# Performance work log

Measured on AMD Instinct MI355X. Metric: run time of the kernel, lower is better.

Reference implementation:

```python
import jax, jax.numpy as jnp
import numpy as np

E = 1_000_000
C_IN = 11
H = 64
N_LAYERS = 4
LN_EPS = 1e-5


def setup_inputs() -> dict:
    key = jax.random.key(0)
    ks = jax.random.split(key, 12)
    x = jax.random.normal(ks[0], (E, C_IN), dtype=jnp.float32)
    neighbors = jax.random.randint(ks[1], (E, 4), 0, E)
    s0 = 1.0 / np.sqrt(5 * C_IN)
    s1 = 1.0 / np.sqrt(5 * H)
    w0 = jax.random.uniform(ks[2], (5 * C_IN, H), jnp.float32, -s0, s0)
    b0 = jax.random.uniform(ks[3], (H,), jnp.float32, -s0, s0)
    w_rest = jax.random.uniform(ks[4], (N_LAYERS - 1, 5 * H, H), jnp.float32, -s1, s1)
    b_rest = jax.random.uniform(ks[5], (N_LAYERS - 1, H), jnp.float32, -s1, s1)
    ln_g = jnp.ones((N_LAYERS, H), jnp.float32)
    ln_b = jnp.zeros((N_LAYERS, H), jnp.float32)
    sc1 = 1.0 / np.sqrt(H)
    sc2 = 1.0 / np.sqrt(H // 2)
    cw1 = jax.random.uniform(ks[6], (H, H // 2), jnp.float32, -sc1, sc1)
    cb1 = jax.random.uniform(ks[7], (H // 2,), jnp.float32, -sc1, sc1)
    cw2 = jax.random.uniform(ks[8], (H // 2, 1), jnp.float32, -sc2, sc2)
    cb2 = jax.random.uniform(ks[9], (1,), jnp.float32, -sc2, sc2)
    return {"x": x, "neighbors": neighbors, "w0": w0, "b0": b0,
            "w_rest": w_rest, "b_rest": b_rest, "ln_g": ln_g, "ln_b": ln_b,
            "cw1": cw1, "cb1": cb1, "cw2": cw2, "cb2": cb2}


def _mesh_conv(x, neighbors, W, b):
    # Gather 4-ring neighbor features: [E,4,C]
    n = x[neighbors]
    a, bb, c, d = n[:, 0], n[:, 1], n[:, 2], n[:, 3]
    # Symmetric MeshCNN features -> 5*C, then linear projection.
    feats = jnp.concatenate([x, jnp.abs(a - c), a + c, jnp.abs(bb - d), bb + d], axis=-1)
    return feats @ W + b


def _layernorm(h, g, b):
    mu = jnp.mean(h, axis=-1, keepdims=True)
    var = jnp.var(h, axis=-1, keepdims=True)
    return (h - mu) * jax.lax.rsqrt(var + LN_EPS) * g + b


def reference(x, neighbors, w0, b0, w_rest, b_rest, ln_g, ln_b, cw1, cb1, cw2, cb2):
    # Layer 0 (no residual; dropout is identity in eval mode)
    h = jax.nn.relu(_layernorm(_mesh_conv(x, neighbors, w0, b0), ln_g[0], ln_b[0]))
    x = h
    for i in range(1, N_LAYERS):
        h = _mesh_conv(x, neighbors, w_rest[i - 1], b_rest[i - 1])
        h = jax.nn.relu(_layernorm(h, ln_g[i], ln_b[i]))
        x = h + x  # residual from layer 2 onward (shapes match)
    z = jax.nn.relu(x @ cw1 + cb1)
    logits = (z @ cw2 + cb2).squeeze(-1)
    return logits
```

## Files before the change

### kernel.cpp

```cpp
#include <hip/hip_runtime.h>
#include <hip/hip_bf16.h>
#include <math.h>

#define E_EDGES 1000000
#define LN_EPS  1e-5f

typedef unsigned short u16;
typedef __bf16 bf16x8 __attribute__((ext_vector_type(8)));
typedef float  f32x16 __attribute__((ext_vector_type(16)));

__device__ __forceinline__ float lo2f(unsigned d) {
    union { unsigned u; float f; } v; v.u = d << 16; return v.f;
}
__device__ __forceinline__ float hi2f(unsigned d) {
    union { unsigned u; float f; } v; v.u = d & 0xffff0000u; return v.f;
}
__device__ __forceinline__ float bf2f(u16 u) {
    union { unsigned u; float f; } v; v.u = ((unsigned)u) << 16; return v.f;
}
__device__ __forceinline__ unsigned pk2(float lo, float hi) {
    __hip_bfloat162 h = __float22bfloat162_rn(make_float2(lo, hi));
    unsigned r; __builtin_memcpy(&r, &h, 4); return r;
}

__global__ __launch_bounds__(256) void wconv_kernel(
    const float* __restrict__ wr, const float* __restrict__ w0,
    const float* __restrict__ cw1, u16* __restrict__ wf)
{
    const int s = blockIdx.x * 256 + threadIdx.x;
    if (s >= 8448) return;
    const int l    = s & 63;
    const int half = l >> 5;
    uint4 pk;
    if (s < 3 * 2560) {
        const int col = ((s >> 6) & 1) * 32 + (l & 31);
        const int L  = s / 2560;
        const int sl = s % 2560;
        const int kb = (sl >> 7) * 16 + half * 8;
        const float* W = wr + L * 320 * 64;
        pk.x = pk2(W[(kb+0)*64+col], W[(kb+1)*64+col]);
        pk.y = pk2(W[(kb+2)*64+col], W[(kb+3)*64+col]);
        pk.z = pk2(W[(kb+4)*64+col], W[(kb+5)*64+col]);
        pk.w = pk2(W[(kb+6)*64+col], W[(kb+7)*64+col]);
    } else if (s < 8192) {
        const int col = ((s >> 6) & 1) * 32 + (l & 31);
        const int sl = s - 3 * 2560;
        const int kb = (sl >> 7) * 16 + half * 8;
        float v[8];
        #pragma unroll
        for (int p = 0; p < 8; ++p) v[p] = (kb + p < 55) ? w0[(kb+p)*64 + col] : 0.f;
        pk.x = pk2(v[0],v[1]); pk.y = pk2(v[2],v[3]);
        pk.z = pk2(v[4],v[5]); pk.w = pk2(v[6],v[7]);
    } else {
        const int sl = s - 8192;
        const int ks = sl >> 6;
        const int col = l & 31;
        const int kb = ks * 16 + half * 8;
        pk.x = pk2(cw1[(kb+0)*32+col], cw1[(kb+1)*32+col]);
        pk.y = pk2(cw1[(kb+2)*32+col], cw1[(kb+3)*32+col]);
        pk.z = pk2(cw1[(kb+4)*32+col], cw1[(kb+5)*32+col]);
        pk.w = pk2(cw1[(kb+6)*32+col], cw1[(kb+7)*32+col]);
    }
    *(uint4*)&wf[(size_t)s * 8] = pk;
}

__global__ __launch_bounds__(256) void xprep_kernel(
    const float* __restrict__ x, u16* __restrict__ xc)
{
    __shared__ float xs[2816];
    const int t = threadIdx.x;
    const long long i0 = (long long)blockIdx.x * 704;
    #pragma unroll
    for (int k = 0; k < 3; ++k) {
        const int idx = t + k * 256;
        if (idx < 704 && i0 + idx < 2750000)
            *(float4*)&xs[idx * 4] = ((const float4*)x)[i0 + idx];
    }
    __syncthreads();
    const size_t e = (size_t)blockIdx.x * 256 + t;
    if (e < E_EDGES) {
        const float* r = &xs[t * 11];
        uint4 o0, o1;
        o0.x = pk2(r[0], r[1]);  o0.y = pk2(r[2], r[3]);
        o0.z = pk2(r[4], r[5]);  o0.w = pk2(r[6], r[7]);
        o1.x = pk2(r[8], r[9]);  o1.y = pk2(r[10], 0.f);
        o1.z = 0u;               o1.w = 0u;
        *(uint4*)&xc[e * 16]     = o0;
        *(uint4*)&xc[e * 16 + 8] = o1;
    }
}

__global__ __launch_bounds__(256, 4) void layer0_mfma(
    const u16* __restrict__ xc, const int* __restrict__ nbr,
    const u16* __restrict__ wf0, const float* __restrict__ bias,
    const float* __restrict__ lng, const float* __restrict__ lnb,
    u16* __restrict__ xout)
{
    __shared__ float smem[64 * 68];
    __shared__ u16  raw[64 * 5 * 16];
    u16* afrag = (u16*)smem;
    const int t  = threadIdx.x;
    const int l  = t & 63;
    const int wv = t >> 6;
    const int e0 = blockIdx.x * 64;
    const int el = t >> 2, cq = t & 3;

    {
        const size_t e = (size_t)(e0 + el);
        const int4 n = *(const int4*)(nbr + 4 * e);
        const int nj = (cq == 0) ? n.x : (cq == 1) ? n.y : (cq == 2) ? n.z : n.w;
        const u16* nr = xc + (size_t)nj * 16;
        u16* dst = raw + (el * 5 + 1 + cq) * 16;
        *(uint4*)dst       = *(const uint4*)nr;
        *(uint4*)(dst + 8) = *(const uint4*)(nr + 8);
        if (cq == 0) {
            const u16* xr = xc + e * 16;
            u16* od = raw + (el * 5) * 16;
            *(uint4*)od       = *(const uint4*)xr;
            *(uint4*)(od + 8) = *(const uint4*)(xr + 8);
        }
    }
    __syncthreads();

    {
        const u16* R = raw + el * 5 * 16;
        float f[16];
        if (cq == 0) {
            #pragma unroll
            for (int i = 0; i < 11; ++i) f[i] = bf2f(R[i]);
            #pragma unroll
            for (int i = 0; i < 5; ++i) f[11+i] = fabsf(bf2f(R[16+i]) - bf2f(R[48+i]));
        } else if (cq == 1) {
            #pragma unroll
            for (int i = 0; i < 6; ++i) f[i] = fabsf(bf2f(R[16+5+i]) - bf2f(R[48+5+i]));
            #pragma unroll
            for (int i = 0; i < 10; ++i) f[6+i] = bf2f(R[16+i]) + bf2f(R[48+i]);
        } else if (cq == 2) {
            f[0] = bf2f(R[16+10]) + bf2f(R[48+10]);
            #pragma unroll
            for (int i = 0; i < 11; ++i) f[1+i] = fabsf(bf2f(R[32+i]) - bf2f(R[64+i]));
            #pragma unroll
            for (int i = 0; i < 4; ++i) f[12+i] = bf2f(R[32+i]) + bf2f(R[64+i]);
        } else {
            #pragma unroll
            for (int i = 0; i < 7; ++i) f[i] = bf2f(R[32+4+i]) + bf2f(R[64+4+i]);
            #pragma unroll
            for (int i = 7; i < 16; ++i) f[i] = 0.f;
        }
        const int mt_g  = el >> 5;
        const int lane0 = el & 31;
        u16* abase = afrag + (size_t)mt_g * (4 * 64 * 8);
        #pragma unroll
        for (int hh = 0; hh < 2; ++hh) {
            uint4 pk;
            pk.x = pk2(f[hh*8+0], f[hh*8+1]);
            pk.y = pk2(f[hh*8+2], f[hh*8+3]);
            pk.z = pk2(f[hh*8+4], f[hh*8+5]);
            pk.w = pk2(f[hh*8+6], f[hh*8+7]);
            const int gsw = (lane0 + 32 * hh) ^ cq;
            *(uint4*)(abase + (size_t)(cq * 64 + gsw) * 8) = pk;
        }
    }
    __syncthreads();

    const int mt = wv >> 1, nt = wv & 1;
    f32x16 acc = {};
    const u16* ab = afrag + (size_t)mt * (4 * 512);
    const u16* bb = wf0 + (size_t)(nt * 64 + l) * 8;
    #pragma unroll
    for (int ks = 0; ks < 4; ++ks) {
        const bf16x8 a8 = *(const bf16x8*)(ab + (size_t)(ks * 64 + (l ^ ks)) * 8);
        const bf16x8 b8 = *(const bf16x8*)(bb + ks * 1024);
        acc = __builtin_amdgcn_mfma_f32_32x32x16_bf16(a8, b8, acc, 0, 0, 0);
    }
    __syncthreads();

    float* ebuf = smem;
    {
        const int col  = nt * 32 + (l & 31);
        const int quad = l >> 5;
        const float bc = bias[col];
        #pragma unroll
        for (int r = 0; r < 16; ++r) {
            const int row = mt * 32 + (r & 3) + 8 * (r >> 2) + 4 * quad;
            ebuf[row * 68 + col] = acc[r] + bc;
        }
    }
    __syncthreads();

    {
        const float* rp = ebuf + el * 68 + cq * 16;
        float v[16];
        float s = 0.f, qs = 0.f;
        #pragma unroll
        for (int i = 0; i < 16; ++i) { v[i] = rp[i]; s += v[i]; qs += v[i] * v[i]; }
        s  += __shfl_xor(s, 1);  s  += __shfl_xor(s, 2);
        qs += __shfl_xor(qs, 1); qs += __shfl_xor(qs, 2);
        const float mu   = s * (1.f / 64.f);
        const float var  = qs * (1.f / 64.f) - mu * mu;
        const float rinv = rsqrtf(var + LN_EPS);
        const size_t e   = (size_t)(e0 + el);
        u16* outp        = xout + e * 64 + cq * 16;
        #pragma unroll
        for (int h = 0; h < 2; ++h) {
            uint4 o; unsigned* op = (unsigned*)&o;
            #pragma unroll
            for (int i = 0; i < 4; ++i) {
                const int ci = cq * 16 + h * 8 + i * 2;
                const float y0 = fmaxf(fmaf((v[h*8+i*2]   - mu) * rinv, lng[ci],   lnb[ci]),   0.f);
                const float y1 = fmaxf(fmaf((v[h*8+i*2+1] - mu) * rinv, lng[ci+1], lnb[ci+1]), 0.f);
                op[i] = pk2(y0, y1);
            }
            *(uint4*)(outp + h * 8) = o;
        }
    }
}

__device__ __forceinline__ void layer_gather_pack(
    const u16* __restrict__ xin, const int* __restrict__ nbr,
    u16* __restrict__ afrag, int e0, int el, int cq, uint4& xv0, uint4& xv1)
{
    const size_t e = (size_t)(e0 + el);
    const int4 n = *(const int4*)(nbr + 4 * e);
    const u16* xr = xin + e * 64           + cq * 16;
    const u16* ar = xin + (size_t)n.x * 64 + cq * 16;
    const u16* br = xin + (size_t)n.y * 64 + cq * 16;
    const u16* cr = xin + (size_t)n.z * 64 + cq * 16;
    const u16* dr = xin + (size_t)n.w * 64 + cq * 16;
    xv0 = *(const uint4*)(xr);                 xv1 = *(const uint4*)(xr + 8);
    const uint4 av0 = *(const uint4*)(ar);     const uint4 av1 = *(const uint4*)(ar + 8);
    const uint4 bv0 = *(const uint4*)(br);     const uint4 bv1 = *(const uint4*)(br + 8);
    const uint4 cv0 = *(const uint4*)(cr);     const uint4 cv1 = *(const uint4*)(cr + 8);
    const uint4 dv0 = *(const uint4*)(dr);     const uint4 dv1 = *(const uint4*)(dr + 8);
    const int mt_g  = el >> 5;
    const int lane0 = el & 31;
    u16* abase = afrag + (size_t)mt_g * (20 * 64 * 8);
    #pragma unroll
    for (int w8 = 0; w8 < 2; ++w8) {
        const uint4 xv = w8 ? xv1 : xv0;
        const uint4 av = w8 ? av1 : av0;
        const uint4 bv = w8 ? bv1 : bv0;
        const uint4 cv = w8 ? cv1 : cv0;
        const uint4 dv = w8 ? dv1 : dv0;
        const int gsw = (lane0 + 32 * w8) ^ cq;
        uint4 g1, g2, g3, g4;
        const unsigned* ap = (const unsigned*)&av;
        const unsigned* bp = (const unsigned*)&bv;
        const unsigned* cp = (const unsigned*)&cv;
        const unsigned* dp = (const unsigned*)&dv;
        unsigned* g1p = (unsigned*)&g1; unsigned* g2p = (unsigned*)&g2;
        unsigned* g3p = (unsigned*)&g3; unsigned* g4p = (unsigned*)&g4;
        #pragma unroll
        for (int i = 0; i < 4; ++i) {
            const float a0 = lo2f(ap[i]), a1 = hi2f(ap[i]);
            const float c0 = lo2f(cp[i]), c1 = hi2f(cp[i]);
            g1p[i] = pk2(a0 - c0, a1 - c1) & 0x7FFF7FFFu;
            g2p[i] = pk2(a0 + c0, a1 + c1);
            const float b0 = lo2f(bp[i]), b1 = hi2f(bp[i]);
            const float d0 = lo2f(dp[i]), d1 = hi2f(dp[i]);
            g3p[i] = pk2(b0 - d0, b1 - d1) & 0x7FFF7FFFu;
            g4p[i] = pk2(b0 + d0, b1 + d1);
        }
        *(uint4*)(abase + (size_t)(((0*4 + cq) * 64) + gsw) * 8) = xv;
        *(uint4*)(abase + (size_t)(((1*4 + cq) * 64) + gsw) * 8) = g1;
        *(uint4*)(abase + (size_t)(((2*4 + cq) * 64) + gsw) * 8) = g2;
        *(uint4*)(abase + (size_t)(((3*4 + cq) * 64) + gsw) * 8) = g3;
        *(uint4*)(abase + (size_t)(((4*4 + cq) * 64) + gsw) * 8) = g4;
    }
}

__global__ __launch_bounds__(256, 4) void layer_mfma(
    const u16* __restrict__ xin, const int* __restrict__ nbr,
    const u16* __restrict__ wf, const float* __restrict__ bias,
    const float* __restrict__ lng, const float* __restrict__ lnb,
    u16* __restrict__ xout)
{
    __shared__ u16 afrag[2 * 20 * 64 * 8];
    const int t  = threadIdx.x;
    const int l  = t & 63;
    const int wv = t >> 6;
    const int e0 = blockIdx.x * 64;
    const int el = t >> 2;
    const int cq = t & 3;

    float lgv[16], lbv[16];
    #pragma unroll
    for (int j = 0; j < 4; ++j) {
        *(float4*)&lgv[j * 4] = *(const float4*)(lng + cq * 16 + j * 4);
        *(float4*)&lbv[j * 4] = *(const float4*)(lnb + cq * 16 + j * 4);
    }

    uint4 xv0, xv1;
    layer_gather_pack(xin, nbr, afrag, e0, el, cq, xv0, xv1);
    __syncthreads();

    const int mt = wv >> 1, nt = wv & 1;
    f32x16 acc = {};
    const u16* ab = afrag + (size_t)mt * (20 * 512);
    const u16* bb = wf + (size_t)(nt * 64 + l) * 8;
    #pragma unroll
    for (int ks = 0; ks < 20; ++ks) {
        const bf16x8 a8 = *(const bf16x8*)(ab + (size_t)(ks * 64 + (l ^ (ks & 3))) * 8);
        const bf16x8 b8 = *(const bf16x8*)(bb + ks * 1024);
        acc = __builtin_amdgcn_mfma_f32_32x32x16_bf16(a8, b8, acc, 0, 0, 0);
    }
    __syncthreads();

    float* ebuf = (float*)afrag;
    {
        const int col  = nt * 32 + (l & 31);
        const int quad = l >> 5;
        const float bc = bias[col];
        #pragma unroll
        for (int r = 0; r < 16; ++r) {
            const int row = mt * 32 + (r & 3) + 8 * (r >> 2) + 4 * quad;
            ebuf[row * 68 + col] = acc[r] + bc;
        }
    }
    __syncthreads();

    {
        const float* rp = ebuf + el * 68 + cq * 16;
        float v[16];
        float s = 0.f, qs = 0.f;
        #pragma unroll
        for (int i = 0; i < 16; ++i) { v[i] = rp[i]; s += v[i]; qs += v[i] * v[i]; }
        s  += __shfl_xor(s, 1);  s  += __shfl_xor(s, 2);
        qs += __shfl_xor(qs, 1); qs += __shfl_xor(qs, 2);
        const float mu   = s * (1.f / 64.f);
        const float var  = qs * (1.f / 64.f) - mu * mu;
        const float rinv = rsqrtf(var + LN_EPS);
        const size_t e   = (size_t)(e0 + el);
        u16* outp        = xout + e * 64 + cq * 16;
        #pragma unroll
        for (int h = 0; h < 2; ++h) {
            const uint4 res = h ? xv1 : xv0;
            const unsigned* rr = (const unsigned*)&res;
            uint4 o; unsigned* op = (unsigned*)&o;
            #pragma unroll
            for (int i = 0; i < 4; ++i) {
                const int k = h * 8 + i * 2;
                const float y0 = fmaxf(fmaf((v[k]   - mu) * rinv, lgv[k],   lbv[k]),   0.f) + lo2f(rr[i]);
                const float y1 = fmaxf(fmaf((v[k+1] - mu) * rinv, lgv[k+1], lbv[k+1]), 0.f) + hi2f(rr[i]);
                op[i] = pk2(y0, y1);
            }
            *(uint4*)(outp + h * 8) = o;
        }
    }
}

__global__ __launch_bounds__(256, 4) void layer_head_mfma(
    const u16* __restrict__ xin, const int* __restrict__ nbr,
    const u16* __restrict__ wf, const float* __restrict__ bias,
    const float* __restrict__ lng, const float* __restrict__ lnb,
    const u16* __restrict__ wfh, const float* __restrict__ cb1,
    const float* __restrict__ cw2, const float* __restrict__ cb2,
    float* __restrict__ out)
{
    __shared__ u16 afrag[2 * 20 * 64 * 8];
    u16*   ybuf  = afrag + 9216;
    float* hbuf2 = (float*)(afrag + 14336);
    const int t  = threadIdx.x;
    const int l  = t & 63;
    const int wv = t >> 6;
    const int e0 = blockIdx.x * 64;
    const int el = t >> 2;
    const int cq = t & 3;

    float lgv[16], lbv[16];
    #pragma unroll
    for (int j = 0; j < 4; ++j) {
        *(float4*)&lgv[j * 4] = *(const float4*)(lng + cq * 16 + j * 4);
        *(float4*)&lbv[j * 4] = *(const float4*)(lnb + cq * 16 + j * 4);
    }

    uint4 xv0, xv1;
    layer_gather_pack(xin, nbr, afrag, e0, el, cq, xv0, xv1);
    __syncthreads();

    const int mt = wv >> 1, nt = wv & 1;
    f32x16 acc = {};
    {
        const u16* ab = afrag + (size_t)mt * (20 * 512);
        const u16* bb = wf + (size_t)(nt * 64 + l) * 8;
        #pragma unroll
        for (int ks = 0; ks < 20; ++ks) {
            const bf16x8 a8 = *(const bf16x8*)(ab + (size_t)(ks * 64 + (l ^ (ks & 3))) * 8);
            const bf16x8 b8 = *(const bf16x8*)(bb + ks * 1024);
            acc = __builtin_amdgcn_mfma_f32_32x32x16_bf16(a8, b8, acc, 0, 0, 0);
        }
    }
    __syncthreads();

    float* ebuf = (float*)afrag;
    {
        const int col  = nt * 32 + (l & 31);
        const int quad = l >> 5;
        const float bc = bias[col];
        #pragma unroll
        for (int r = 0; r < 16; ++r) {
            const int row = mt * 32 + (r & 3) + 8 * (r >> 2) + 4 * quad;
            ebuf[row * 68 + col] = acc[r] + bc;
        }
    }
    __syncthreads();

    {
        const float* rp = ebuf + el * 68 + cq * 16;
        float v[16];
        float s = 0.f, qs = 0.f;
        #pragma unroll
        for (int i = 0; i < 16; ++i) { v[i] = rp[i]; s += v[i]; qs += v[i] * v[i]; }
        s  += __shfl_xor(s, 1);  s  += __shfl_xor(s, 2);
        qs += __shfl_xor(qs, 1); qs += __shfl_xor(qs, 2);
        const float mu   = s * (1.f / 64.f);
        const float var  = qs * (1.f / 64.f) - mu * mu;
        const float rinv = rsqrtf(var + LN_EPS);
        const int mt_g  = el >> 5;
        const int lane0 = el & 31;
        #pragma unroll
        for (int h = 0; h < 2; ++h) {
            const uint4 res = h ? xv1 : xv0;
            const unsigned* rr = (const unsigned*)&res;
            uint4 o; unsigned* op = (unsigned*)&o;
            #pragma unroll
            for (int i = 0; i < 4; ++i) {
                const int k = h * 8 + i * 2;
                const float y0 = fmaxf(fmaf((v[k]   - mu) * rinv, lgv[k],   lbv[k]),   0.f) + lo2f(rr[i]);
                const float y1 = fmaxf(fmaf((v[k+1] - mu) * rinv, lgv[k+1], lbv[k+1]), 0.f) + hi2f(rr[i]);
                op[i] = pk2(y0, y1);
            }
            const int gsw = (lane0 + 32 * h) ^ cq;
            *(uint4*)(ybuf + (size_t)(((mt_g * 4 + cq) * 64) + gsw) * 8) = o;
        }
    }
    __syncthreads();

    if (wv < 2) {
        const int mt2 = wv;
        f32x16 a2 = {};
        #pragma unroll
        for (int ks = 0; ks < 4; ++ks) {
            const bf16x8 a8 = *(const bf16x8*)(ybuf + (size_t)(((mt2 * 4 + ks) * 64) + (l ^ ks)) * 8);
            const bf16x8 b8 = *(const bf16x8*)(wfh + (size_t)(ks * 64 + l) * 8);
            a2 = __builtin_amdgcn_mfma_f32_32x32x16_bf16(a8, b8, a2, 0, 0, 0);
        }
        const int col = l & 31;
        const float bc1 = cb1[col];
        const float w2v = cw2[col];
        float* hb = hbuf2 + mt2 * (32 * 33);
        #pragma unroll
        for (int r = 0; r < 16; ++r) {
            const int row = (r & 3) + 8 * (r >> 2) + 4 * (l >> 5);
            hb[row * 33 + col] = fmaxf(a2[r] + bc1, 0.f) * w2v;
        }
    }
    __syncthreads();

    if (t < 128) {
        const int edge = t >> 1, part = t & 1;
        const float* rp = hbuf2 + (edge >> 5) * (32 * 33) + (edge & 31) * 33 + part * 16;
        float s = 0.f;
        #pragma unroll
        for (int i = 0; i < 16; ++i) s += rp[i];
        s += __shfl_xor(s, 1);
        if (part == 0) out[e0 + edge] = s + cb2[0];
    }
}

__global__ __launch_bounds__(256) void head_mfma(
    const u16* __restrict__ xin,
    const float* __restrict__ cw1, const float* __restrict__ cb1,
    const float* __restrict__ cw2, const float* __restrict__ cb2,
    float* __restrict__ out)
{
    __shared__ float hbuf[4][32 * 33];
    const int t    = threadIdx.x;
    const int l    = t & 63;
    const int wv   = t >> 6;
    const int col  = l & 31;
    const int half = l >> 5;

    bf16x8 bf[4];
    #pragma unroll
    for (int ks = 0; ks < 4; ++ks) {
        const int kb = ks * 16 + half * 8;
        uint4 pk;
        pk.x = pk2(cw1[(kb+0)*32 + col], cw1[(kb+1)*32 + col]);
        pk.y = pk2(cw1[(kb+2)*32 + col], cw1[(kb+3)*32 + col]);
        pk.z = pk2(cw1[(kb+4)*32 + col], cw1[(kb+5)*32 + col]);
        pk.w = pk2(cw1[(kb+6)*32 + col], cw1[(kb+7)*32 + col]);
        __builtin_memcpy(&bf[ks], &pk, 16);
    }
    const float bc = cb1[col];
    const float w2 = cw2[col];
    const float b2 = cb2[0];

    int tile = blockIdx.x * 4 + wv;
    const int valid = tile < (E_EDGES / 32);
    if (!valid) tile = E_EDGES / 32 - 1;
    const size_t e0 = (size_t)tile * 32;
    const u16* xb = xin + (e0 + col) * 64 + half * 8;
    f32x16 acc = {};
    #pragma unroll
    for (int ks = 0; ks < 4; ++ks) {
        const bf16x8 a8 = *(const bf16x8*)(xb + ks * 16);
        acc = __builtin_amdgcn_mfma_f32_32x32x16_bf16(a8, bf[ks], acc, 0, 0, 0);
    }
    float* hb = hbuf[wv];
    #pragma unroll
    for (int r = 0; r < 16; ++r) {
        const int row = (r & 3) + 8 * (r >> 2) + 4 * half;
        hb[row * 33 + col] = fmaxf(acc[r] + bc, 0.f) * w2;
    }
    __syncthreads();
    const int row2 = l >> 1, part = l & 1;
    const float* rp = hb + row2 * 33 + part * 16;
    float s = 0.f;
    #pragma unroll
    for (int i = 0; i < 16; ++i) s += rp[i];
    s += __shfl_xor(s, 1);
    if (valid && part == 0) out[e0 + row2] = s + b2;
}

extern "C" void kernel_launch(void* const* d_in, const int* in_sizes, int n_in,
                              void* d_out, int out_size, void* d_ws, size_t ws_size,
                              hipStream_t stream)
{
// ... 41 lines not shown
```

Measured before the change: 645.1 us.

## Make each wave own 16 edges with 16x16x32 MFMA and wave-local sync

Restructures the mesh-conv layer kernels so that each wavefront processes its own 16 edges end to end. Each wave keeps a private LDS slice and computes all 64 output columns with 16x16x32 bf16 MFMAs instead of four waves sharing 32x32 tiles. Block-wide __syncthreads are replaced by wave-local lgkmcnt waits, and the weight prepacking is reordered to the new fragment layout. The head reduction now uses cross-lane shuffles instead of an LDS pass. This removes inter-wave barrier stalls. In exchange, every wave reloads the full weight fragments from global memory and the XOR LDS swizzle is dropped, so bank conflicts may appear.

```diff
diff --git a/kernel.cpp b/kernel.cpp
--- a/kernel.cpp
+++ b/kernel.cpp
@@ -7,7 +7,13 @@
 
 typedef unsigned short u16;
 typedef __bf16 bf16x8 __attribute__((ext_vector_type(8)));
-typedef float  f32x16 __attribute__((ext_vector_type(16)));
+typedef float  f32x4  __attribute__((ext_vector_type(4)));
+
+#define WAVE_SYNC() do {                                      \
+    __builtin_amdgcn_sched_barrier(0);                        \
+    asm volatile("s_waitcnt lgkmcnt(0)" ::: "memory");        \
+    __builtin_amdgcn_sched_barrier(0);                        \
+} while (0)
 
 __device__ __forceinline__ float lo2f(unsigned d) {
     union { unsigned u; float f; } v; v.u = d << 16; return v.f;
@@ -30,36 +36,42 @@
     const int s = blockIdx.x * 256 + threadIdx.x;
     if (s >= 8448) return;
     const int l    = s & 63;
-    const int half = l >> 5;
+    const int colb = l & 15;
+    const int k0   = (l >> 4) * 8;
     uint4 pk;
     if (s < 3 * 2560) {
-        const int col = ((s >> 6) & 1) * 32 + (l & 31);
         const int L  = s / 2560;
         const int sl = s % 2560;
-        const int kb = (sl >> 7) * 16 + half * 8;
+        const int ks = sl >> 8;
+        const int nt = (sl >> 6) & 3;
+        const int k  = 32 * ks + k0;
+        const int col = nt * 16 + colb;
         const float* W = wr + L * 320 * 64;
-        pk.x = pk2(W[(kb+0)*64+col], W[(kb+1)*64+col]);
-        pk.y = pk2(W[(kb+2)*64+col], W[(kb+3)*64+col]);
-        pk.z = pk2(W[(kb+4)*64+col], W[(kb+5)*64+col]);
-        pk.w = pk2(W[(kb+6)*64+col], W[(kb+7)*64+col]);
+        pk.x = pk2(W[(k+0)*64+col], W[(k+1)*64+col]);
+        pk.y = pk2(W[(k+2)*64+col], W[(k+3)*64+col]);
+        pk.z = pk2(W[(k+4)*64+col], W[(k+5)*64+col]);
+        pk.w = pk2(W[(k+6)*64+col], W[(k+7)*64+col]);
     } else if (s < 8192) {
-        const int col = ((s >> 6) & 1) * 32 + (l & 31);
         const int sl = s - 3 * 2560;
-        const int kb = (sl >> 7) * 16 + half * 8;
+        const int ks = sl >> 8;
+        const int nt = (sl >> 6) & 3;
+        const int k  = 32 * ks + k0;
+        const int col = nt * 16 + colb;
         float v[8];
         #pragma unroll
-        for (int p = 0; p < 8; ++p) v[p] = (kb + p < 55) ? w0[(kb+p)*64 + col] : 0.f;
+        for (int p = 0; p < 8; ++p) v[p] = (k + p < 55) ? w0[(k+p)*64 + col] : 0.f;
         pk.x = pk2(v[0],v[1]); pk.y = pk2(v[2],v[3]);
         pk.z = pk2(v[4],v[5]); pk.w = pk2(v[6],v[7]);
     } else {
         const int sl = s - 8192;
-        const int ks = sl >> 6;
-        const int col = l & 31;
-        const int kb = ks * 16 + half * 8;
-        pk.x = pk2(cw1[(kb+0)*32+col], cw1[(kb+1)*32+col]);
-        pk.y = pk2(cw1[(kb+2)*32+col], cw1[(kb+3)*32+col]);
-        pk.z = pk2(cw1[(kb+4)*32+col], cw1[(kb+5)*32+col]);
-        pk.w = pk2(cw1[(kb+6)*32+col], cw1[(kb+7)*32+col]);
+        const int ks = sl >> 7;
+        const int nt = (sl >> 6) & 1;
+        const int k  = 32 * ks + k0;
+        const int col = nt * 16 + colb;
+        pk.x = pk2(cw1[(k+0)*32+col], cw1[(k+1)*32+col]);
+        pk.y = pk2(cw1[(k+2)*32+col], cw1[(k+3)*32+col]);
+        pk.z = pk2(cw1[(k+4)*32+col], cw1[(k+5)*32+col]);
+        pk.w = pk2(cw1[(k+6)*32+col], cw1[(k+7)*32+col]);
     }
     *(uint4*)&wf[(size_t)s * 8] = pk;
 }
@@ -96,17 +108,17 @@
     const float* __restrict__ lng, const float* __restrict__ lnb,
     u16* __restrict__ xout)
 {
-    __shared__ float smem[64 * 68];
-    __shared__ u16  raw[64 * 5 * 16];
-    u16* afrag = (u16*)smem;
+    __shared__ u16 lds[4 * 2304];
     const int t  = threadIdx.x;
     const int l  = t & 63;
     const int wv = t >> 6;
-    const int e0 = blockIdx.x * 64;
-    const int el = t >> 2, cq = t & 3;
-
-    {
-        const size_t e = (size_t)(e0 + el);
+    u16* raw = lds + wv * 2304;
+    u16* aw  = raw + 1280;
+    const int el = l >> 2, cq = l & 3;
+    const int e0w = blockIdx.x * 64 + wv * 16;
+
+    {
+        const size_t e = (size_t)e0w + el;
         const int4 n = *(const int4*)(nbr + 4 * e);
         const int nj = (cq == 0) ? n.x : (cq == 1) ? n.y : (cq == 2) ? n.z : n.w;
         const u16* nr = xc + (size_t)nj * 16;
@@ -115,15 +127,15 @@
         *(uint4*)(dst + 8) = *(const uint4*)(nr + 8);
         if (cq == 0) {
             const u16* xr = xc + e * 16;
-            u16* od = raw + (el * 5) * 16;
+            u16* od = raw + el * 5 * 16;
             *(uint4*)od       = *(const uint4*)xr;
-            *(uint4*)(od + 8) = *(const uint4*)(xr + 8);
-        }
-    }
-    __syncthreads();
-
-    {
-        const u16* R = raw + el * 5 * 16;
+            *(uint4*)(od + 8) = *(const uint4*)(nr - nr + xr + 8);
+        }
+    }
+    WAVE_SYNC();
+
+    {
+        const u16* R = raw + el * 80;
         float f[16];
         if (cq == 0) {
             #pragma unroll
@@ -147,49 +159,47 @@
             #pragma unroll
             for (int i = 7; i < 16; ++i) f[i] = 0.f;
         }
-        const int mt_g  = el >> 5;
-        const int lane0 = el & 31;
-        u16* abase = afrag + (size_t)mt_g * (4 * 64 * 8);
-        #pragma unroll
-        for (int hh = 0; hh < 2; ++hh) {
+        const int base = (cq >> 1) * 64 + (cq & 1) * 32 + el;
+        #pragma unroll
+        for (int h = 0; h < 2; ++h) {
             uint4 pk;
-            pk.x = pk2(f[hh*8+0], f[hh*8+1]);
-            pk.y = pk2(f[hh*8+2], f[hh*8+3]);
-            pk.z = pk2(f[hh*8+4], f[hh*8+5]);
-            pk.w = pk2(f[hh*8+6], f[hh*8+7]);
-            const int gsw = (lane0 + 32 * hh) ^ cq;
-            *(uint4*)(abase + (size_t)(cq * 64 + gsw) * 8) = pk;
-        }
-    }
-    __syncthreads();
-
-    const int mt = wv >> 1, nt = wv & 1;
-    f32x16 acc = {};
-    const u16* ab = afrag + (size_t)mt * (4 * 512);
-    const u16* bb = wf0 + (size_t)(nt * 64 + l) * 8;
-    #pragma unroll
-    for (int ks = 0; ks < 4; ++ks) {
-        const bf16x8 a8 = *(const bf16x8*)(ab + (size_t)(ks * 64 + (l ^ ks)) * 8);
-        const bf16x8 b8 = *(const bf16x8*)(bb + ks * 1024);
-        acc = __builtin_amdgcn_mfma_f32_32x32x16_bf16(a8, b8, acc, 0, 0, 0);
-    }
-    __syncthreads();
-
-    float* ebuf = smem;
-    {
-        const int col  = nt * 32 + (l & 31);
-        const int quad = l >> 5;
-        const float bc = bias[col];
-        #pragma unroll
-        for (int r = 0; r < 16; ++r) {
-            const int row = mt * 32 + (r & 3) + 8 * (r >> 2) + 4 * quad;
-            ebuf[row * 68 + col] = acc[r] + bc;
-        }
-    }
-    __syncthreads();
-
-    {
-        const float* rp = ebuf + el * 68 + cq * 16;
+            pk.x = pk2(f[h*8+0], f[h*8+1]);
+            pk.y = pk2(f[h*8+2], f[h*8+3]);
+            pk.z = pk2(f[h*8+4], f[h*8+5]);
+            pk.w = pk2(f[h*8+6], f[h*8+7]);
+            *(uint4*)(aw + (size_t)(base + h * 16) * 8) = pk;
+        }
+    }
+    WAVE_SYNC();
+
+    f32x4 ac0 = {}, ac1 = {}, ac2 = {}, ac3 = {};
+    #pragma unroll
+    for (int ks = 0; ks < 2; ++ks) {
+        const bf16x8 a8 = *(const bf16x8*)(aw + (size_t)(ks * 64 + l) * 8);
+        const u16* bk = wf0 + (size_t)(ks * 256 + l) * 8;
+        ac0 = __builtin_amdgcn_mfma_f32_16x16x32_bf16(a8, *(const bf16x8*)(bk       ), ac0, 0, 0, 0);
+        ac1 = __builtin_amdgcn_mfma_f32_16x16x32_bf16(a8, *(const bf16x8*)(bk +  512), ac1, 0, 0, 0);
+        ac2 = __builtin_amdgcn_mfma_f32_16x16x32_bf16(a8, *(const bf16x8*)(bk + 1024), ac2, 0, 0, 0);
+        ac3 = __builtin_amdgcn_mfma_f32_16x16x32_bf16(a8, *(const bf16x8*)(bk + 1536), ac3, 0, 0, 0);
+    }
+    WAVE_SYNC();
+
+    float* ew = (float*)raw;
+    const int colb = l & 15, rb = (l >> 4) * 4;
+    {
+        const float b0 = bias[colb],      b1 = bias[16 + colb];
+        const float b2 = bias[32 + colb], b3 = bias[48 + colb];
+        #pragma unroll
+        for (int r = 0; r < 4; ++r) {
+            float* er = ew + (rb + r) * 67;
+            er[colb]      = ac0[r] + b0;  er[16 + colb] = ac1[r] + b1;
+            er[32 + colb] = ac2[r] + b2;  er[48 + colb] = ac3[r] + b3;
+        }
+    }
+    WAVE_SYNC();
+
+    {
+        const float* rp = ew + el * 67 + cq * 16;
         float v[16];
         float s = 0.f, qs = 0.f;
         #pragma unroll
@@ -199,7 +209,7 @@
         const float mu   = s * (1.f / 64.f);
         const float var  = qs * (1.f / 64.f) - mu * mu;
         const float rinv = rsqrtf(var + LN_EPS);
-        const size_t e   = (size_t)(e0 + el);
+        const size_t e   = (size_t)e0w + el;
         u16* outp        = xout + e * 64 + cq * 16;
         #pragma unroll
         for (int h = 0; h < 2; ++h) {
@@ -216,11 +226,11 @@
     }
 }
 
-__device__ __forceinline__ void layer_gather_pack(
+__device__ __forceinline__ void gather_pack16(
     const u16* __restrict__ xin, const int* __restrict__ nbr,
-    u16* __restrict__ afrag, int e0, int el, int cq, uint4& xv0, uint4& xv1)
-{
-    const size_t e = (size_t)(e0 + el);
+    u16* __restrict__ aw, int e0w, int el, int cq, uint4& xv0, uint4& xv1)
+{
+    const size_t e = (size_t)e0w + el;
     const int4 n = *(const int4*)(nbr + 4 * e);
     const u16* xr = xin + e * 64           + cq * 16;
     const u16* ar = xin + (size_t)n.x * 64 + cq * 16;
@@ -232,17 +242,14 @@
     const uint4 bv0 = *(const uint4*)(br);     const uint4 bv1 = *(const uint4*)(br + 8);
     const uint4 cv0 = *(const uint4*)(cr);     const uint4 cv1 = *(const uint4*)(cr + 8);
     const uint4 dv0 = *(const uint4*)(dr);     const uint4 dv1 = *(const uint4*)(dr + 8);
-    const int mt_g  = el >> 5;
-    const int lane0 = el & 31;
-    u16* abase = afrag + (size_t)mt_g * (20 * 64 * 8);
-    #pragma unroll
-    for (int w8 = 0; w8 < 2; ++w8) {
-        const uint4 xv = w8 ? xv1 : xv0;
-        const uint4 av = w8 ? av1 : av0;
-        const uint4 bv = w8 ? bv1 : bv0;
-        const uint4 cv = w8 ? cv1 : cv0;
-        const uint4 dv = w8 ? dv1 : dv0;
-        const int gsw = (lane0 + 32 * w8) ^ cq;
+    const int base = (cq >> 1) * 64 + (cq & 1) * 32 + el;
+    #pragma unroll
+    for (int h = 0; h < 2; ++h) {
+        const uint4 xv = h ? xv1 : xv0;
+        const uint4 av = h ? av1 : av0;
+        const uint4 bv = h ? bv1 : bv0;
+        const uint4 cv = h ? cv1 : cv0;
+        const uint4 dv = h ? dv1 : dv0;
         uint4 g1, g2, g3, g4;
         const unsigned* ap = (const unsigned*)&av;
         const unsigned* bp = (const unsigned*)&bv;
@@ -261,11 +268,12 @@
             g3p[i] = pk2(b0 - d0, b1 - d1) & 0x7FFF7FFFu;
             g4p[i] = pk2(b0 + d0, b1 + d1);
         }
-        *(uint4*)(abase + (size_t)(((0*4 + cq) * 64) + gsw) * 8) = xv;
-        *(uint4*)(abase + (size_t)(((1*4 + cq) * 64) + gsw) * 8) = g1;
-        *(uint4*)(abase + (size_t)(((2*4 + cq) * 64) + gsw) * 8) = g2;
-        *(uint4*)(abase + (size_t)(((3*4 + cq) * 64) + gsw) * 8) = g3;
-        *(uint4*)(abase + (size_t)(((4*4 + cq) * 64) + gsw) * 8) = g4;
+        u16* w = aw + (size_t)(base + h * 16) * 8;
+        *(uint4*)(w)           = xv;
+        *(uint4*)(w + 128 * 8) = g1;
+        *(uint4*)(w + 256 * 8) = g2;
+        *(uint4*)(w + 384 * 8) = g3;
+        *(uint4*)(w + 512 * 8) = g4;
     }
 }
 
@@ -275,52 +283,52 @@
     const float* __restrict__ lng, const float* __restrict__ lnb,
     u16* __restrict__ xout)
 {
-    __shared__ u16 afrag[2 * 20 * 64 * 8];
+    __shared__ u16 lds[4 * 5120];
     const int t  = threadIdx.x;
     const int l  = t & 63;
     const int wv = t >> 6;
-    const int e0 = blockIdx.x * 64;
-    const int el = t >> 2;
-    const int cq = t & 3;
-
-    float lgv[16], lbv[16];
-    #pragma unroll
-    for (int j = 0; j < 4; ++j) {
-        *(float4*)&lgv[j * 4] = *(const float4*)(lng + cq * 16 + j * 4);
-        *(float4*)&lbv[j * 4] = *(const float4*)(lnb + cq * 16 + j * 4);
-    }
+    u16* aw = lds + wv * 5120;
+    const int el = l >> 2, cq = l & 3;
+    const int e0w = blockIdx.x * 64 + wv * 16;
 
     uint4 xv0, xv1;
-    layer_gather_pack(xin, nbr, afrag, e0, el, cq, xv0, xv1);
-    __syncthreads();
-
-    const int mt = wv >> 1, nt = wv & 1;
-    f32x16 acc = {};
-    const u16* ab = afrag + (size_t)mt * (20 * 512);
-    const u16* bb = wf + (size_t)(nt * 64 + l) * 8;
-    #pragma unroll
-    for (int ks = 0; ks < 20; ++ks) {
-        const bf16x8 a8 = *(const bf16x8*)(ab + (size_t)(ks * 64 + (l ^ (ks & 3))) * 8);
-        const bf16x8 b8 = *(const bf16x8*)(bb + ks * 1024);
-        acc = __builtin_amdgcn_mfma_f32_32x32x16_bf16(a8, b8, acc, 0, 0, 0);
-    }
-    __syncthreads();
-
-    float* ebuf = (float*)afrag;
-    {
-        const int col  = nt * 32 + (l & 31);
-        const int quad = l >> 5;
-        const float bc = bias[col];
-        #pragma unroll
-        for (int r = 0; r < 16; ++r) {
-            const int row = mt * 32 + (r & 3) + 8 * (r >> 2) + 4 * quad;
-            ebuf[row * 68 + col] = acc[r] + bc;
-        }
-    }
-    __syncthreads();
-
-    {
-        const float* rp = ebuf + el * 68 + cq * 16;
+    gather_pack16(xin, nbr, aw, e0w, el, cq, xv0, xv1);
+    WAVE_SYNC();
+
+    f32x4 ac0 = {}, ac1 = {}, ac2 = {}, ac3 = {};
+    #pragma unroll
+    for (int ks = 0; ks < 10; ++ks) {
+        const bf16x8 a8 = *(const bf16x8*)(aw + (size_t)(ks * 64 + l) * 8);
+        const u16* bk = wf + (size_t)(ks * 256 + l) * 8;
+        ac0 = __builtin_amdgcn_mfma_f32_16x16x32_bf16(a8, *(const bf16x8*)(bk       ), ac0, 0, 0, 0);
+        ac1 = __builtin_amdgcn_mfma_f32_16x16x32_bf16(a8, *(const bf16x8*)(bk +  512), ac1, 0, 0, 0);
+        ac2 = __builtin_amdgcn_mfma_f32_16x16x32_bf16(a8, *(const bf16x8*)(bk + 1024), ac2, 0, 0, 0);
+        ac3 = __builtin_amdgcn_mfma_f32_16x16x32_bf16(a8, *(const bf16x8*)(bk + 1536), ac3, 0, 0, 0);
+    }
+    WAVE_SYNC();
+
+    float* ew = (float*)aw;
+    const int colb = l & 15, rb = (l >> 4) * 4;
+    {
+        const float b0 = bias[colb],      b1 = bias[16 + colb];
+        const float b2 = bias[32 + colb], b3 = bias[48 + colb];
+        #pragma unroll
+        for (int r = 0; r < 4; ++r) {
+            float* er = ew + (rb + r) * 67;
+            er[colb]      = ac0[r] + b0;  er[16 + colb] = ac1[r] + b1;
+            er[32 + colb] = ac2[r] + b2;  er[48 + colb] = ac3[r] + b3;
+        }
+    }
+    WAVE_SYNC();
+
+    {
+        float lgv[16], lbv[16];
+        #pragma unroll
+        for (int j = 0; j < 4; ++j) {
+            *(float4*)&lgv[j * 4] = *(const float4*)(lng + cq * 16 + j * 4);
+            *(float4*)&lbv[j * 4] = *(const float4*)(lnb + cq * 16 + j * 4);
+        }
+        const float* rp = ew + el * 67 + cq * 16;
         float v[16];
         float s = 0.f, qs = 0.f;
         #pragma unroll
@@ -330,7 +338,7 @@
         const float mu   = s * (1.f / 64.f);
         const float var  = qs * (1.f / 64.f) - mu * mu;
         const float rinv = rsqrtf(var + LN_EPS);
-        const size_t e   = (size_t)(e0 + el);
+        const size_t e   = (size_t)e0w + el;
         u16* outp        = xout + e * 64 + cq * 16;
         #pragma unroll
         for (int h = 0; h < 2; ++h) {
@@ -357,56 +365,53 @@
     const float* __restrict__ cw2, const float* __restrict__ cb2,
     float* __restrict__ out)
 {
-    __shared__ u16 afrag[2 * 20 * 64 * 8];
-    u16*   ybuf  = afrag + 9216;
-    float* hbuf2 = (float*)(afrag + 14336);
+    __shared__ u16 lds[4 * 5120];
     const int t  = threadIdx.x;
     const int l  = t & 63;
     const int wv = t >> 6;
-    const int e0 = blockIdx.x * 64;
-    const int el = t >> 2;
-    const int cq = t & 3;
-
-    float lgv[16], lbv[16];
-    #pragma unroll
-    for (int j = 0; j < 4; ++j) {
-        *(float4*)&lgv[j * 4] = *(const float4*)(lng + cq * 16 + j * 4);
-        *(float4*)&lbv[j * 4] = *(const float4*)(lnb + cq * 16 + j * 4);
-    }
+    u16* aw = lds + wv * 5120;
+    u16* yb = aw + 2176;
+    const int el = l >> 2, cq = l & 3;
+    const int e0w = blockIdx.x * 64 + wv * 16;
 
     uint4 xv0, xv1;
-    layer_gather_pack(xin, nbr, afrag, e0, el, cq, xv0, xv1);
-    __syncthreads();
-
-    const int mt = wv >> 1, nt = wv & 1;
-    f32x16 acc = {};
-    {
-        const u16* ab = afrag + (size_t)mt * (20 * 512);
-        const u16* bb = wf + (size_t)(nt * 64 + l) * 8;
-        #pragma unroll
-        for (int ks = 0; ks < 20; ++ks) {
-            const bf16x8 a8 = *(const bf16x8*)(ab + (size_t)(ks * 64 + (l ^ (ks & 3))) * 8);
-            const bf16x8 b8 = *(const bf16x8*)(bb + ks * 1024);
-            acc = __builtin_amdgcn_mfma_f32_32x32x16_bf16(a8, b8, acc, 0, 0, 0);
-        }
-    }
-    __syncthreads();
-
-    float* ebuf = (float*)afrag;
-    {
-        const int col  = nt * 32 + (l & 31);
-        const int quad = l >> 5;
-        const float bc = bias[col];
-        #pragma unroll
-        for (int r = 0; r < 16; ++r) {
-            const int row = mt * 32 + (r & 3) + 8 * (r >> 2) + 4 * quad;
-            ebuf[row * 68 + col] = acc[r] + bc;
-        }
-    }
-    __syncthreads();
-
-    {
-        const float* rp = ebuf + el * 68 + cq * 16;
+    gather_pack16(xin, nbr, aw, e0w, el, cq, xv0, xv1);
+    WAVE_SYNC();
+
+    f32x4 ac0 = {}, ac1 = {}, ac2 = {}, ac3 = {};
+    #pragma unroll
+    for (int ks = 0; ks < 10; ++ks) {
+        const bf16x8 a8 = *(const bf16x8*)(aw + (size_t)(ks * 64 + l) * 8);
+        const u16* bk = wf + (size_t)(ks * 256 + l) * 8;
+        ac0 = __builtin_amdgcn_mfma_f32_16x16x32_bf16(a8, *(const bf16x8*)(bk       ), ac0, 0, 0, 0);
+        ac1 = __builtin_amdgcn_mfma_f32_16x16x32_bf16(a8, *(const bf16x8*)(bk +  512), ac1, 0, 0, 0);
+        ac2 = __builtin_amdgcn_mfma_f32_16x16x32_bf16(a8, *(const bf16x8*)(bk + 1024), ac2, 0, 0, 0);
+        ac3 = __builtin_amdgcn_mfma_f32_16x16x32_bf16(a8, *(const bf16x8*)(bk + 1536), ac3, 0, 0, 0);
+    }
+    WAVE_SYNC();
+
+    float* ew = (float*)aw;
+    const int colb = l & 15, rb = (l >> 4) * 4;
+    {
+        const float b0 = bias[colb],      b1 = bias[16 + colb];
+        const float b2 = bias[32 + colb], b3 = bias[48 + colb];
+        #pragma unroll
+        for (int r = 0; r < 4; ++r) {
+            float* er = ew + (rb + r) * 67;
+            er[colb]      = ac0[r] + b0;  er[16 + colb] = ac1[r] + b1;
+            er[32 + colb] = ac2[r] + b2;  er[48 + colb] = ac3[r] + b3;
+        }
+    }
+    WAVE_SYNC();
+
+    {
+        float lgv[16], lbv[16];
+        #pragma unroll
+        for (int j = 0; j < 4; ++j) {
+            *(float4*)&lgv[j * 4] = *(const float4*)(lng + cq * 16 + j * 4);
+            *(float4*)&lbv[j * 4] = *(const float4*)(lnb + cq * 16 + j * 4);
+        }
+        const float* rp = ew + el * 67 + cq * 16;
         float v[16];
         float s = 0.f, qs = 0.f;
         #pragma unroll
@@ -416,8 +421,7 @@
         const float mu   = s * (1.f / 64.f);
         const float var  = qs * (1.f / 64.f) - mu * mu;
         const float rinv = rsqrtf(var + LN_EPS);
-        const int mt_g  = el >> 5;
-        const int lane0 = el & 31;
+        const int ybase = (cq >> 1) * 64 + (cq & 1) * 32 + el;
         #pragma unroll
         for (int h = 0; h < 2; ++h) {
             const uint4 res = h ? xv1 : xv0;
@@ -430,41 +434,36 @@
                 const float y1 = fmaxf(fmaf((v[k+1] - mu) * rinv, lgv[k+1], lbv[k+1]), 0.f) + hi2f(rr[i]);
                 op[i] = pk2(y0, y1);
             }
-            const int gsw = (lane0 + 32 * h) ^ cq;
-            *(uint4*)(ybuf + (size_t)(((mt_g * 4 + cq) * 64) + gsw) * 8) = o;
-        }
-    }
-    __syncthreads();
-
-    if (wv < 2) {
-        const int mt2 = wv;
-        f32x16 a2 = {};
-        #pragma unroll
-        for (int ks = 0; ks < 4; ++ks) {
-            const bf16x8 a8 = *(const bf16x8*)(ybuf + (size_t)(((mt2 * 4 + ks) * 64) + (l ^ ks)) * 8);
-            const bf16x8 b8 = *(const bf16x8*)(wfh + (size_t)(ks * 64 + l) * 8);
-            a2 = __builtin_amdgcn_mfma_f32_32x32x16_bf16(a8, b8, a2, 0, 0, 0);
-        }
-        const int col = l & 31;
-        const float bc1 = cb1[col];
-        const float w2v = cw2[col];
-        float* hb = hbuf2 + mt2 * (32 * 33);
-        #pragma unroll
-        for (int r = 0; r < 16; ++r) {
-            const int row = (r & 3) + 8 * (r >> 2) + 4 * (l >> 5);
-            hb[row * 33 + col] = fmaxf(a2[r] + bc1, 0.f) * w2v;
-        }
-    }
-    __syncthreads();
-
-    if (t < 128) {
-        const int edge = t >> 1, part = t & 1;
-        const float* rp = hbuf2 + (edge >> 5) * (32 * 33) + (edge & 31) * 33 + part * 16;
-        float s = 0.f;
-        #pragma unroll
-        for (int i = 0; i < 16; ++i) s += rp[i];
-        s += __shfl_xor(s, 1);
-        if (part == 0) out[e0 + edge] = s + cb2[0];
+            *(uint4*)(yb + (size_t)(ybase + h * 16) * 8) = o;
+        }
+    }
+    WAVE_SYNC();
+
+    f32x4 h0 = {}, h1 = {};
+    #pragma unroll
+    for (int ks = 0; ks < 2; ++ks) {
+        const bf16x8 a8 = *(const bf16x8*)(yb + (size_t)(ks * 64 + l) * 8);
+        const u16* bk = wfh + (size_t)(ks * 128 + l) * 8;
+        h0 = __builtin_amdgcn_mfma_f32_16x16x32_bf16(a8, *(const bf16x8*)(bk      ), h0, 0, 0, 0);
+        h1 = __builtin_amdgcn_mfma_f32_16x16x32_bf16(a8, *(const bf16x8*)(bk + 512), h1, 0, 0, 0);
+    }
+    {
+        const float q1 = cb1[colb], q2 = cb1[16 + colb];
+        const float w1 = cw2[colb], w2 = cw2[16 + colb];
+        float sr[4];
+        #pragma unroll
+        for (int r = 0; r < 4; ++r)
+            sr[r] = fmaxf(h0[r] + q1, 0.f) * w1 + fmaxf(h1[r] + q2, 0.f) * w2;
+        #pragma unroll
+        for (int m = 1; m < 16; m <<= 1) {
+            #pragma unroll
+            for (int r = 0; r < 4; ++r) sr[r] += __shfl_xor(sr[r], m);
+        }
+        if (colb == 0) {
+            const float b2v = cb2[0];
+            #pragma unroll
+            for (int r = 0; r < 4; ++r) out[e0w + rb + r] = sr[r] + b2v;
+        }
     }
 }
 
@@ -474,6 +473,7 @@
     const float* __restrict__ cw2, const float* __restrict__ cb2,
     float* __restrict__ out)
 {
+    typedef float f32x16 __attribute__((ext_vector_type(16)));
     __shared__ float hbuf[4][32 * 33];
     const int t    = threadIdx.x;
     const int l    = t & 63;
```

Result: slower. 693.7 us (+7.5%).

## Split A-fragment staging into two K phases to shrink LDS footprint

Applied to the files above, without the earlier changes.

The layer kernels now stage the MFMA A operand in two phases: x plus the a/c features (12 k-steps) first, then the b/d features (8 k-steps) reuse the same shared buffer after a barrier. This cuts shared memory per block from 40 KB to about 24–25 KB, which may let more blocks reside per CU for this latency-bound gather workload. The LayerNorm gamma/beta loads are also moved to just before use to shorten register live ranges. In exchange there are two extra block barriers, and the b/d neighbor values stay live in registers across the first MFMA phase.

```diff
diff --git a/kernel.cpp b/kernel.cpp
--- a/kernel.cpp
+++ b/kernel.cpp
@@ -216,10 +216,37 @@
     }
 }
 
-__device__ __forceinline__ void layer_gather_pack(
+__device__ __forceinline__ void feat_pair(
+    const uint4 u, const uint4 w, uint4& gd, uint4& gs)
+{
+    const unsigned* up = (const unsigned*)&u;
+    const unsigned* wp = (const unsigned*)&w;
+    unsigned* dp = (unsigned*)&gd;
+    unsigned* sp = (unsigned*)&gs;
+    #pragma unroll
+    for (int i = 0; i < 4; ++i) {
+        const float u0 = lo2f(up[i]), u1 = hi2f(up[i]);
+        const float w0 = lo2f(wp[i]), w1 = hi2f(wp[i]);
+        dp[i] = pk2(u0 - w0, u1 - w1) & 0x7FFF7FFFu;
+        sp[i] = pk2(u0 + w0, u1 + w1);
+    }
+}
+
+__global__ __launch_bounds__(256, 4) void layer_mfma(
     const u16* __restrict__ xin, const int* __restrict__ nbr,
-    u16* __restrict__ afrag, int e0, int el, int cq, uint4& xv0, uint4& xv1)
-{
+    const u16* __restrict__ wf, const float* __restrict__ bias,
+    const float* __restrict__ lng, const float* __restrict__ lnb,
+    u16* __restrict__ xout)
+{
+    __shared__ u16 afrag[2 * 12 * 64 * 8];
+    const int t  = threadIdx.x;
+    const int l  = t & 63;
+    const int wv = t >> 6;
+    const int e0 = blockIdx.x * 64;
+    const int el = t >> 2;
+    const int cq = t & 3;
+    const int mt = wv >> 1, nt = wv & 1;
+
     const size_t e = (size_t)(e0 + el);
     const int4 n = *(const int4*)(nbr + 4 * e);
     const u16* xr = xin + e * 64           + cq * 16;
@@ -227,85 +254,60 @@
     const u16* br = xin + (size_t)n.y * 64 + cq * 16;
     const u16* cr = xin + (size_t)n.z * 64 + cq * 16;
     const u16* dr = xin + (size_t)n.w * 64 + cq * 16;
-    xv0 = *(const uint4*)(xr);                 xv1 = *(const uint4*)(xr + 8);
+    const uint4 xv0 = *(const uint4*)(xr);     const uint4 xv1 = *(const uint4*)(xr + 8);
     const uint4 av0 = *(const uint4*)(ar);     const uint4 av1 = *(const uint4*)(ar + 8);
     const uint4 bv0 = *(const uint4*)(br);     const uint4 bv1 = *(const uint4*)(br + 8);
     const uint4 cv0 = *(const uint4*)(cr);     const uint4 cv1 = *(const uint4*)(cr + 8);
     const uint4 dv0 = *(const uint4*)(dr);     const uint4 dv1 = *(const uint4*)(dr + 8);
+
     const int mt_g  = el >> 5;
     const int lane0 = el & 31;
-    u16* abase = afrag + (size_t)mt_g * (20 * 64 * 8);
-    #pragma unroll
-    for (int w8 = 0; w8 < 2; ++w8) {
-        const uint4 xv = w8 ? xv1 : xv0;
-        const uint4 av = w8 ? av1 : av0;
-        const uint4 bv = w8 ? bv1 : bv0;
-        const uint4 cv = w8 ? cv1 : cv0;
-        const uint4 dv = w8 ? dv1 : dv0;
-        const int gsw = (lane0 + 32 * w8) ^ cq;
-        uint4 g1, g2, g3, g4;
-        const unsigned* ap = (const unsigned*)&av;
-        const unsigned* bp = (const unsigned*)&bv;
-        const unsigned* cp = (const unsigned*)&cv;
-        const unsigned* dp = (const unsigned*)&dv;
-        unsigned* g1p = (unsigned*)&g1; unsigned* g2p = (unsigned*)&g2;
-        unsigned* g3p = (unsigned*)&g3; unsigned* g4p = (unsigned*)&g4;
-        #pragma unroll
-        for (int i = 0; i < 4; ++i) {
-            const float a0 = lo2f(ap[i]), a1 = hi2f(ap[i]);
-            const float c0 = lo2f(cp[i]), c1 = hi2f(cp[i]);
-            g1p[i] = pk2(a0 - c0, a1 - c1) & 0x7FFF7FFFu;
-            g2p[i] = pk2(a0 + c0, a1 + c1);
-            const float b0 = lo2f(bp[i]), b1 = hi2f(bp[i]);
-            const float d0 = lo2f(dp[i]), d1 = hi2f(dp[i]);
-            g3p[i] = pk2(b0 - d0, b1 - d1) & 0x7FFF7FFFu;
-            g4p[i] = pk2(b0 + d0, b1 + d1);
-        }
-        *(uint4*)(abase + (size_t)(((0*4 + cq) * 64) + gsw) * 8) = xv;
-        *(uint4*)(abase + (size_t)(((1*4 + cq) * 64) + gsw) * 8) = g1;
-        *(uint4*)(abase + (size_t)(((2*4 + cq) * 64) + gsw) * 8) = g2;
-        *(uint4*)(abase + (size_t)(((3*4 + cq) * 64) + gsw) * 8) = g3;
-        *(uint4*)(abase + (size_t)(((4*4 + cq) * 64) + gsw) * 8) = g4;
-    }
-}
-
-__global__ __launch_bounds__(256, 4) void layer_mfma(
-    const u16* __restrict__ xin, const int* __restrict__ nbr,
-    const u16* __restrict__ wf, const float* __restrict__ bias,
-    const float* __restrict__ lng, const float* __restrict__ lnb,
-    u16* __restrict__ xout)
-{
-    __shared__ u16 afrag[2 * 20 * 64 * 8];
-    const int t  = threadIdx.x;
-    const int l  = t & 63;
-    const int wv = t >> 6;
-    const int e0 = blockIdx.x * 64;
-    const int el = t >> 2;
-    const int cq = t & 3;
-
-    float lgv[16], lbv[16];
-    #pragma unroll
-    for (int j = 0; j < 4; ++j) {
-        *(float4*)&lgv[j * 4] = *(const float4*)(lng + cq * 16 + j * 4);
-        *(float4*)&lbv[j * 4] = *(const float4*)(lnb + cq * 16 + j * 4);
-    }
-
-    uint4 xv0, xv1;
-    layer_gather_pack(xin, nbr, afrag, e0, el, cq, xv0, xv1);
-    __syncthreads();
-
-    const int mt = wv >> 1, nt = wv & 1;
+    u16* abase = afrag + (size_t)mt_g * (12 * 512);
+
+    {
+        #pragma unroll
+        for (int w8 = 0; w8 < 2; ++w8) {
+            const int gsw = (lane0 + 32 * w8) ^ cq;
+            uint4 g1, g2;
+            feat_pair(w8 ? av1 : av0, w8 ? cv1 : cv0, g1, g2);
+            *(uint4*)(abase + (size_t)(((0*4 + cq) * 64) + gsw) * 8) = w8 ? xv1 : xv0;
+            *(uint4*)(abase + (size_t)(((1*4 + cq) * 64) + gsw) * 8) = g1;
+            *(uint4*)(abase + (size_t)(((2*4 + cq) * 64) + gsw) * 8) = g2;
+        }
+    }
+    __syncthreads();
+
     f32x16 acc = {};
-    const u16* ab = afrag + (size_t)mt * (20 * 512);
+    const u16* ab = afrag + (size_t)mt * (12 * 512);
     const u16* bb = wf + (size_t)(nt * 64 + l) * 8;
     #pragma unroll
-    for (int ks = 0; ks < 20; ++ks) {
+    for (int ks = 0; ks < 12; ++ks) {
         const bf16x8 a8 = *(const bf16x8*)(ab + (size_t)(ks * 64 + (l ^ (ks & 3))) * 8);
         const bf16x8 b8 = *(const bf16x8*)(bb + ks * 1024);
         acc = __builtin_amdgcn_mfma_f32_32x32x16_bf16(a8, b8, acc, 0, 0, 0);
     }
     __syncthreads();
 
+    {
+        #pragma unroll
+        for (int w8 = 0; w8 < 2; ++w8) {
+            const int gsw = (lane0 + 32 * w8) ^ cq;
+            uint4 g3, g4;
+            feat_pair(w8 ? bv1 : bv0, w8 ? dv1 : dv0, g3, g4);
+            *(uint4*)(abase + (size_t)(((0*4 + cq) * 64) + gsw) * 8) = g3;
+            *(uint4*)(abase + (size_t)(((1*4 + cq) * 64) + gsw) * 8) = g4;
+        }
+    }
+    __syncthreads();
+
+    #pragma unroll
+    for (int ks = 0; ks < 8; ++ks) {
+        const bf16x8 a8 = *(const bf16x8*)(ab + (size_t)(ks * 64 + (l ^ (ks & 3))) * 8);
+        const bf16x8 b8 = *(const bf16x8*)(bb + (12 + ks) * 1024);
+        acc = __builtin_amdgcn_mfma_f32_32x32x16_bf16(a8, b8, acc, 0, 0, 0);
+    }
+    __syncthreads();
+
     float* ebuf = (float*)afrag;
     {
         const int col  = nt * 32 + (l & 31);
@@ -320,6 +322,12 @@
     __syncthreads();
 
     {
+        float lgv[16], lbv[16];
+        #pragma unroll
+        for (int j = 0; j < 4; ++j) {
+            *(float4*)&lgv[j * 4] = *(const float4*)(lng + cq * 16 + j * 4);
+            *(float4*)&lbv[j * 4] = *(const float4*)(lnb + cq * 16 + j * 4);
+        }
         const float* rp = ebuf + el * 68 + cq * 16;
         float v[16];
         float s = 0.f, qs = 0.f;
@@ -330,7 +338,6 @@
         const float mu   = s * (1.f / 64.f);
         const float var  = qs * (1.f / 64.f) - mu * mu;
         const float rinv = rsqrtf(var + LN_EPS);
-        const size_t e   = (size_t)(e0 + el);
         u16* outp        = xout + e * 64 + cq * 16;
         #pragma unroll
         for (int h = 0; h < 2; ++h) {
@@ -357,38 +364,76 @@
     const float* __restrict__ cw2, const float* __restrict__ cb2,
     float* __restrict__ out)
 {
-    __shared__ u16 afrag[2 * 20 * 64 * 8];
-    u16*   ybuf  = afrag + 9216;
-    float* hbuf2 = (float*)(afrag + 14336);
+    __shared__ u16 lds[12800];
+    u16*   afrag = lds;
+    u16*   ybuf  = lds + 8704;
+    float* hbuf2 = (float*)lds;
     const int t  = threadIdx.x;
     const int l  = t & 63;
     const int wv = t >> 6;
     const int e0 = blockIdx.x * 64;
     const int el = t >> 2;
     const int cq = t & 3;
-
-    float lgv[16], lbv[16];
-    #pragma unroll
-    for (int j = 0; j < 4; ++j) {
-        *(float4*)&lgv[j * 4] = *(const float4*)(lng + cq * 16 + j * 4);
-        *(float4*)&lbv[j * 4] = *(const float4*)(lnb + cq * 16 + j * 4);
-    }
-
-    uint4 xv0, xv1;
-    layer_gather_pack(xin, nbr, afrag, e0, el, cq, xv0, xv1);
-    __syncthreads();
-
     const int mt = wv >> 1, nt = wv & 1;
+
+    const size_t e = (size_t)(e0 + el);
+    const int4 n = *(const int4*)(nbr + 4 * e);
+    const u16* xr = xin + e * 64           + cq * 16;
+    const u16* ar = xin + (size_t)n.x * 64 + cq * 16;
+    const u16* br = xin + (size_t)n.y * 64 + cq * 16;
+    const u16* cr = xin + (size_t)n.z * 64 + cq * 16;
+    const u16* dr = xin + (size_t)n.w * 64 + cq * 16;
+    const uint4 xv0 = *(const uint4*)(xr);     const uint4 xv1 = *(const uint4*)(xr + 8);
+    const uint4 av0 = *(const uint4*)(ar);     const uint4 av1 = *(const uint4*)(ar + 8);
+    const uint4 bv0 = *(const uint4*)(br);     const uint4 bv1 = *(const uint4*)(br + 8);
+    const uint4 cv0 = *(const uint4*)(cr);     const uint4 cv1 = *(const uint4*)(cr + 8);
+    const uint4 dv0 = *(const uint4*)(dr);     const uint4 dv1 = *(const uint4*)(dr + 8);
+
+    const int mt_g  = el >> 5;
+    const int lane0 = el & 31;
+    u16* abase = afrag + (size_t)mt_g * (12 * 512);
+
+    {
+        #pragma unroll
+        for (int w8 = 0; w8 < 2; ++w8) {
+            const int gsw = (lane0 + 32 * w8) ^ cq;
+            uint4 g1, g2;
+            feat_pair(w8 ? av1 : av0, w8 ? cv1 : cv0, g1, g2);
+            *(uint4*)(abase + (size_t)(((0*4 + cq) * 64) + gsw) * 8) = w8 ? xv1 : xv0;
+            *(uint4*)(abase + (size_t)(((1*4 + cq) * 64) + gsw) * 8) = g1;
+            *(uint4*)(abase + (size_t)(((2*4 + cq) * 64) + gsw) * 8) = g2;
+        }
+    }
+    __syncthreads();
+
     f32x16 acc = {};
-    {
-        const u16* ab = afrag + (size_t)mt * (20 * 512);
-        const u16* bb = wf + (size_t)(nt * 64 + l) * 8;
-        #pragma unroll
-        for (int ks = 0; ks < 20; ++ks) {
-            const bf16x8 a8 = *(const bf16x8*)(ab + (size_t)(ks * 64 + (l ^ (ks & 3))) * 8);
-            const bf16x8 b8 = *(const bf16x8*)(bb + ks * 1024);
-            acc = __builtin_amdgcn_mfma_f32_32x32x16_bf16(a8, b8, acc, 0, 0, 0);
-        }
+    const u16* ab = afrag + (size_t)mt * (12 * 512);
+    const u16* bb = wf + (size_t)(nt * 64 + l) * 8;
+    #pragma unroll
+    for (int ks = 0; ks < 12; ++ks) {
+        const bf16x8 a8 = *(const bf16x8*)(ab + (size_t)(ks * 64 + (l ^ (ks & 3))) * 8);
+        const bf16x8 b8 = *(const bf16x8*)(bb + ks * 1024);
+        acc = __builtin_amdgcn_mfma_f32_32x32x16_bf16(a8, b8, acc, 0, 0, 0);
+    }
+    __syncthreads();
+
+    {
+        #pragma unroll
+        for (int w8 = 0; w8 < 2; ++w8) {
+            const int gsw = (lane0 + 32 * w8) ^ cq;
+            uint4 g3, g4;
+            feat_pair(w8 ? bv1 : bv0, w8 ? dv1 : dv0, g3, g4);
+            *(uint4*)(abase + (size_t)(((0*4 + cq) * 64) + gsw) * 8) = g3;
+            *(uint4*)(abase + (size_t)(((1*4 + cq) * 64) + gsw) * 8) = g4;
+        }
+    }
+    __syncthreads();
+
+    #pragma unroll
+    for (int ks = 0; ks < 8; ++ks) {
+        const bf16x8 a8 = *(const bf16x8*)(ab + (size_t)(ks * 64 + (l ^ (ks & 3))) * 8);
+        const bf16x8 b8 = *(const bf16x8*)(bb + (12 + ks) * 1024);
+        acc = __builtin_amdgcn_mfma_f32_32x32x16_bf16(a8, b8, acc, 0, 0, 0);
     }
     __syncthreads();
 
@@ -406,6 +451,12 @@
     __syncthreads();
 
     {
+        float lgv[16], lbv[16];
+        #pragma unroll
+        for (int j = 0; j < 4; ++j) {
+            *(float4*)&lgv[j * 4] = *(const float4*)(lng + cq * 16 + j * 4);
+            *(float4*)&lbv[j * 4] = *(const float4*)(lnb + cq * 16 + j * 4);
+        }
         const float* rp = ebuf + el * 68 + cq * 16;
         float v[16];
         float s = 0.f, qs = 0.f;
@@ -416,8 +467,6 @@
         const float mu   = s * (1.f / 64.f);
         const float var  = qs * (1.f / 64.f) - mu * mu;
         const float rinv = rsqrtf(var + LN_EPS);
-        const int mt_g  = el >> 5;
-        const int lane0 = el & 31;
         #pragma unroll
         for (int h = 0; h < 2; ++h) {
             const uint4 res = h ? xv1 : xv0;
```

New measurement: 583.0 us, median of 2. 9.6% less time.
